# Kernel tuning notes

Measured on AMD Instinct MI355X. Metric: run time of the kernel, lower is better.

The kernel has to match this reference:

```python
import jax, jax.numpy as jnp
import numpy as np

D_MODEL = 768
N_HEADS = 24
D_HEAD = 64
D_STATE = 64
CHUNK = 64
D_INNER = N_HEADS * D_HEAD  # 1536
N_LAYER = 24
B_SZ = 2
SEQ = 8192
RMS_EPS = 1.1920929e-07  # torch.finfo(float32).eps (nn.RMSNorm default eps)


def setup_inputs() -> dict:
    key = jax.random.key(0)
    ks = jax.random.split(key, 8)
    proj = N_HEADS * (1 + 2 * D_STATE)
    return {
        "hidden_states": jax.random.normal(ks[0], (B_SZ, SEQ, D_MODEL), jnp.float32),
        "norm_w": jnp.ones((D_MODEL,), jnp.float32),
        "in_proj_w": jax.random.normal(ks[1], (2 * D_INNER, D_MODEL), jnp.float32) * 0.02,
        "in_proj_b": jnp.zeros((2 * D_INNER,), jnp.float32),
        "conv_w": jax.random.normal(ks[2], (D_INNER, 1, 4), jnp.float32) * 0.25,
        "conv_b": jnp.zeros((D_INNER,), jnp.float32),
        "x_proj_w": jax.random.normal(ks[3], (proj, D_INNER), jnp.float32) * 0.02,
        "x_proj_b": jnp.zeros((proj,), jnp.float32),
        "A_log": jnp.full((N_HEADS,), float(np.log(0.5)), jnp.float32),
        "log2_alpha_base": jnp.full((N_HEADS,), -0.15, jnp.float32),
        "log2_beta": jnp.zeros((N_HEADS,), jnp.float32),
        "surprise_ema": jnp.ones((N_HEADS,), jnp.float32),
        "out_proj_w": jax.random.normal(ks[4], (D_MODEL, D_INNER), jnp.float32) * 0.02,
        "out_proj_b": jnp.zeros((D_MODEL,), jnp.float32),
        "res_gate": jnp.full((1,), 1.0 / float(np.sqrt(2 * N_LAYER)), jnp.float32),
    }


def _block_forward(hidden_states, norm_w, in_proj_w, in_proj_b, conv_w, conv_b,
                   x_proj_w, x_proj_b, A_log, log2_alpha_base, log2_beta,
                   surprise_ema, out_proj_w, out_proj_b, res_gate):
    residual = hidden_states
    b, L, _ = hidden_states.shape

    # RMSNorm
    x = hidden_states * jax.lax.rsqrt(
        jnp.mean(hidden_states ** 2, axis=-1, keepdims=True) + RMS_EPS) * norm_w

    # in_proj, split x/z
    xz = hidden_states_proj = x @ in_proj_w.T + in_proj_b
    x, z = jnp.split(xz, 2, axis=-1)  # [b, L, d_inner] each

    # causal depthwise conv1d (kernel 4, padding 3, then truncate to L)
    xc = jnp.transpose(x, (0, 2, 1))  # [b, C, L]
    xc = jax.lax.conv_general_dilated(
        xc, conv_w, window_strides=(1,), padding=[(3, 3)],
        dimension_numbers=("NCH", "OIH", "NCH"), feature_group_count=D_INNER)
    xc = xc[:, :, :L] + conv_b[None, :, None]
    x = jax.nn.silu(jnp.transpose(xc, (0, 2, 1)))  # [b, L, d_inner]

    # x_proj -> dt, B, C
    xp = (x @ x_proj_w.T + x_proj_b).reshape(b, L, N_HEADS, 1 + 2 * D_STATE)
    dt = xp[..., 0]
    B_ssm = xp[..., 1:1 + D_STATE]
    C_ssm = xp[..., 1 + D_STATE:]
    B_ssm = B_ssm / jnp.maximum(jnp.linalg.norm(B_ssm, axis=-1, keepdims=True), 1e-12)
    C_ssm = C_ssm / jnp.maximum(jnp.linalg.norm(C_ssm, axis=-1, keepdims=True), 1e-12)

    A = jnp.clip(A_log, -2.3, -0.01)[None, None, :]  # [1,1,H]
    dt_scale = jnp.clip(jax.nn.softplus(jnp.clip(dt, -10.0, 10.0)), 0.01, 10.0)
    A = jnp.clip(A * dt_scale, -20.0, -0.001)  # [b, L, H]

    X = x.reshape(b, L, N_HEADS, D_HEAD)

    # ---- chunked surprise-gated SSD (L divisible by CHUNK) ----
    n = L // CHUNK
    X_t = X.reshape(b, n, CHUNK, N_HEADS, D_HEAD).transpose(0, 3, 1, 2, 4)      # b h n c d
    A_t = A.reshape(b, n, CHUNK, N_HEADS).transpose(0, 3, 1, 2)                 # b h n c
    B_t = B_ssm.reshape(b, n, CHUNK, N_HEADS, D_STATE).transpose(0, 3, 1, 2, 4) # b h n c s
    C_t = C_ssm.reshape(b, n, CHUNK, N_HEADS, D_STATE).transpose(0, 3, 1, 2, 4) # b h n c s

    BX = jnp.einsum("bhncs,bhncd->bhnsd", B_t, X_t)
    chunk_surprise = jnp.mean(BX ** 2, axis=(-1, -2))  # [b, h, n]

    # surprise gate (training=True: EMA updated first, no_grad)
    mean_s = jax.lax.stop_gradient(jnp.mean(chunk_surprise, axis=(0, 2)))
    ema = 0.99 * surprise_ema + 0.01 * mean_s
    normalized = chunk_surprise / (ema[None, :, None] + 1e-6)
    alpha_base = 1.0 - 2.0 ** jnp.clip(log2_alpha_base, -3.32, -0.015)  # [H]
    beta = 2.0 ** jnp.clip(log2_beta, -2.0, 2.0)                        # [H]
    boost_pos = jax.nn.relu(jnp.tanh(beta[None, :, None] * normalized))
    ab = alpha_base[None, :, None]
    alpha = jnp.clip(ab + (1.0 - ab) * boost_pos, 0.01, 0.999)          # [b, h, n]

    A_mod = A_t * (1.0 - alpha)[..., None]          # b h n c
    A_cs = jnp.cumsum(A_mod, axis=-1)               # b h n c

    # intra-chunk: L[i,j] = exp(cs_i - cs_j) for i >= j
    diff = A_cs[..., :, None] - A_cs[..., None, :]  # b h n c c
    mask = jnp.tril(jnp.ones((CHUNK, CHUNK), bool))
    Lmat = jnp.where(mask, jnp.exp(diff), 0.0)
    CB = jnp.einsum("bhnid,bhnjd->bhnij", C_t, B_t)
    Y_intra = jnp.einsum("bhnij,bhnjd->bhnid", Lmat * CB, X_t)

    # inter-chunk recurrence
    decay_chunk = jnp.exp(jnp.sum(A_mod, axis=-1))              # b h n
    decay_to_end = jnp.exp(A_cs[..., -1:] - A_cs)               # b h n c
    h_chunk_final = jnp.einsum("bhnc,bhncs,bhncd->bhnsd",
                               decay_to_end, B_t, X_t)           # b h n s d

    def step(carry, inp):
        d, hf = inp  # d: [b,h], hf: [b,h,s,d]
        new = d[..., None, None] * carry + hf
        return new, carry  # emit state BEFORE this chunk

    carry0 = jnp.zeros((b, N_HEADS, D_STATE, D_HEAD), X.dtype)
    _, h_inter = jax.lax.scan(
        step, carry0,
        (decay_chunk.transpose(2, 0, 1), h_chunk_final.transpose(2, 0, 1, 3, 4)))
    h_inter = h_inter.transpose(1, 2, 0, 3, 4)  # b h n s d

    decay_from_start = jnp.exp(A_cs)  # b h n c
    Y_inter = jnp.einsum("bhnis,bhnsp,bhni->bhnip", C_t, h_inter, decay_from_start)

    Y = (Y_intra + Y_inter).transpose(0, 2, 3, 1, 4).reshape(b, L, D_INNER)

    # gate + out proj + gated residual
    y = jnp.clip(Y, -100.0, 100.0) * jax.nn.sigmoid(z)
    out = jnp.clip(y @ out_proj_w.T + out_proj_b, -100.0, 100.0)
    return residual + out * res_gate


def reference(hidden_states, norm_w, in_proj_w, in_proj_b, conv_w, conv_b,
              x_proj_w, x_proj_b, A_log, log2_alpha_base, log2_beta,
              surprise_ema, out_proj_w, out_proj_b, res_gate):
    return _block_forward(hidden_states, norm_w, in_proj_w, in_proj_b, conv_w,
                          conv_b, x_proj_w, x_proj_b, A_log, log2_alpha_base,
                          log2_beta, surprise_ema, out_proj_w, out_proj_b, res_gate)
```

## Files before the change

kernel.cpp:

```cpp
#include <hip/hip_runtime.h>
#include <hip/hip_bf16.h>
#include <cstdint>
#include <cstddef>

#define L_SEQ   8192
#define DMODEL  768
#define NHEADS  24
#define DINNER  1536
#define NPROJ   3096
#define NPROJP  3200
#define NTOK    16384
#define SEG_T   4096
#define NSEG    4
#define SEG_CH  64
#define RMS_EPS 1.1920929e-07f

typedef __hip_bfloat16 bf16;
typedef __attribute__((ext_vector_type(8))) short bf8v;
typedef __attribute__((ext_vector_type(4))) float f4v;

__device__ __forceinline__ float clampf(float x, float lo, float hi) {
    return fminf(fmaxf(x, lo), hi);
}
__device__ __forceinline__ float bf2f(bf16 v) { return __bfloat162float(v); }
__device__ __forceinline__ bf16  f2bf(float v) { return __float2bfloat16(v); }
__device__ __forceinline__ short f2bs(float v) {
    bf16 b = __float2bfloat16(v);
    return *reinterpret_cast<short*>(&b);
}
__device__ __forceinline__ void st1(float* p, float v) { *p = v; }
__device__ __forceinline__ void st1(bf16* p, float v) { *p = f2bf(v); }
__device__ __forceinline__ void st4(float* p, float4 v) { *(float4*)p = v; }
__device__ __forceinline__ void st4(bf16* p, float4 v) {
    p[0] = f2bf(v.x); p[1] = f2bf(v.y); p[2] = f2bf(v.z); p[3] = f2bf(v.w);
}

#define GLOAD16(gsrc, ldst) __builtin_amdgcn_global_load_lds( \
    (const __attribute__((address_space(1))) void*)(gsrc),    \
    (__attribute__((address_space(3))) void*)(ldst), 16, 0, 0)

__global__ __launch_bounds__(256) void k_cvt(const float* __restrict__ s,
                                             bf16* __restrict__ d, int n4) {
    int i = blockIdx.x * 256 + threadIdx.x;
    if (i < n4) {
        float4 v = *(const float4*)&s[i * 4];
        st4(&d[i * 4], v);
    }
}
__global__ __launch_bounds__(256) void k_zero(bf16* __restrict__ d, int n) {
    int i = blockIdx.x * 256 + threadIdx.x;
    if (i < n) d[i] = f2bf(0.f);
}

__global__ __launch_bounds__(256) void k_rmsnorm(const float* __restrict__ hs,
                                                 const float* __restrict__ w,
                                                 bf16* __restrict__ xn) {
    int t = blockIdx.x;
    const float* p = hs + (size_t)t * DMODEL;
    float s = 0.f;
    for (int i = threadIdx.x; i < DMODEL; i += 256) { float v = p[i]; s += v * v; }
    for (int off = 32; off; off >>= 1) s += __shfl_xor(s, off, 64);
    __shared__ float ws4[4];
    int lane = threadIdx.x & 63, wv = threadIdx.x >> 6;
    if (lane == 0) ws4[wv] = s;
    __syncthreads();
    s = ws4[0] + ws4[1] + ws4[2] + ws4[3];
    float r = 1.0f / sqrtf(s * (1.0f / DMODEL) + RMS_EPS);
    bf16* o = xn + (size_t)t * DMODEL;
    for (int i = threadIdx.x; i < DMODEL; i += 256) o[i] = f2bf(p[i] * r * w[i]);
}

template <typename TC, int EPI>
__global__ __launch_bounds__(256) void k_mgemm(const bf16* __restrict__ A,
                                               const bf16* __restrict__ B,
                                               const float* __restrict__ bias,
                                               TC* __restrict__ C,
                                               int M, int N, int K,
                                               const float* __restrict__ resid,
                                               const float* __restrict__ gatep,
                                               bf16* __restrict__ halo) {
    __shared__ short As[2][128 * 32];
    __shared__ short Bs[2][128 * 32];
    int tid = threadIdx.x;
    int lane = tid & 63, w = tid >> 6;

    int gx = gridDim.x, gy = gridDim.y;
    int bid = blockIdx.y * gx + blockIdx.x;
    int xcd = bid & 7, idx = bid >> 3;
    int bys = gy >> 3;
    int gby = bys < 8 ? bys : 8;
    int sg  = idx / (gx * gby);
    int rem = idx - sg * (gx * gby);
    int bx  = rem / gby;
    int byl = rem - bx * gby;
    int by  = xcd * bys + sg * gby + byl;
    int m0 = by * 128, n0 = bx * 128;

    int wm = (w >> 1) << 6, wn = (w & 1) << 6;

    const size_t rowskip = (size_t)16 * K * 2;
    const char* Ag = (const char*)(A + (size_t)(m0 + (w << 5) + (lane >> 2)) * K) + (lane & 3) * 16;
    const char* Bg = (const char*)(B + (size_t)(n0 + (w << 5) + (lane >> 2)) * K) + (lane & 3) * 16;
    short* Al0 = &As[0][(w << 5) * 32];
    short* Bl0 = &Bs[0][(w << 5) * 32];
    short* Al1 = &As[1][(w << 5) * 32];
    short* Bl1 = &Bs[1][(w << 5) * 32];

    f4v acc[4][4];
#pragma unroll
    for (int i = 0; i < 4; ++i)
#pragma unroll
        for (int j = 0; j < 4; ++j) acc[i][j] = (f4v){0.f, 0.f, 0.f, 0.f};

    auto stage = [&](int buf, int k0) {
        size_t kb = (size_t)k0 * 2;
        short* Al = buf ? Al1 : Al0;
        short* Bl = buf ? Bl1 : Bl0;
        GLOAD16(Ag + kb,           Al);
        GLOAD16(Ag + kb + rowskip, Al + 16 * 32);
        GLOAD16(Bg + kb,           Bl);
        GLOAD16(Bg + kb + rowskip, Bl + 16 * 32);
    };

    stage(0, 0);
    int cur = 0;
    int row16 = lane & 15, kg = (lane >> 4) << 3;
    for (int k0 = 0; k0 < K; k0 += 32) {
        __syncthreads();
        if (k0 + 32 < K) stage(cur ^ 1, k0 + 32);
        const short* Ab = As[cur];
        const short* Bb = Bs[cur];
        bf8v af[4], bfv[4];
#pragma unroll
        for (int fm = 0; fm < 4; ++fm)
            af[fm] = *(const bf8v*)&Ab[(wm + (fm << 4) + row16) * 32 + kg];
#pragma unroll
        for (int fn = 0; fn < 4; ++fn)
            bfv[fn] = *(const bf8v*)&Bb[(wn + (fn << 4) + row16) * 32 + kg];
#pragma unroll
        for (int fm = 0; fm < 4; ++fm)
#pragma unroll
            for (int fn = 0; fn < 4; ++fn)
                acc[fm][fn] = __builtin_amdgcn_mfma_f32_16x16x32_bf16(
                    af[fm], bfv[fn], acc[fm][fn], 0, 0, 0);
        cur ^= 1;
    }

    float gate = (EPI == 1) ? *gatep : 0.f;
    int rbase = m0 + wm + ((lane >> 4) << 2);
#pragma unroll
    for (int fn = 0; fn < 4; ++fn) {
        int col = n0 + wn + (fn << 4) + (lane & 15);
        if (col >= N) continue;
        float bc = bias[col];
#pragma unroll
        for (int fm = 0; fm < 4; ++fm) {
#pragma unroll
            for (int r = 0; r < 4; ++r) {
                int row = rbase + (fm << 4) + r;
                float v = acc[fm][fn][r] + bc;
                if (EPI == 1)
                    v = resid[(size_t)row * N + col] + clampf(v, -100.f, 100.f) * gate;
                st1(&C[(size_t)row * N + col], v);
                if (halo && row >= M - 3)
                    halo[(size_t)(row - (M - 3)) * N + col] = f2bf(v);
            }
        }
    }
}

__global__ __launch_bounds__(256) void k_conv_silu(const bf16* __restrict__ x,
                                                   const bf16* __restrict__ xh,
                                                   const float* __restrict__ cw,
                                                   const float* __restrict__ cb,
                                                   bf16* __restrict__ xc,
                                                   int l0) {
    int c = blockIdx.x * 256 + threadIdx.x;
    int r = blockIdx.y;
    int l = l0 + r;
    float acc = cb[c];
#pragma unroll
    for (int k = 0; k < 4; ++k) {
        int lp = l - 3 + k;
        if (lp < 0) continue;
        float v = (lp < l0) ? bf2f(xh[(size_t)(lp - l0 + 3) * DINNER + c])
                            : bf2f(x[(size_t)(lp - l0) * DINNER + c]);
        acc += cw[c * 4 + k] * v;
    }
    float sig = 1.f / (1.f + expf(-acc));
    xc[(size_t)r * DINNER + c] = f2bf(acc * sig);
}

__global__ __launch_bounds__(256) void k_prep(const bf16* __restrict__ xp,
                                              const float* __restrict__ A_log,
                                              float* __restrict__ Aarr,
                                              float* __restrict__ invB,
                                              float* __restrict__ invC) {
    int wv = threadIdx.x >> 6, lane = threadIdx.x & 63;
    int idx = blockIdx.x * 4 + wv;
    int t = idx / 24, h = idx - t * 24;
    const bf16* base = xp + (size_t)t * NPROJ + h * 129;
    float b = bf2f(base[1 + lane]), c = bf2f(base[65 + lane]);
    float sb = b * b, sc = c * c;
    for (int off = 32; off; off >>= 1) {
        sb += __shfl_xor(sb, off, 64);
        sc += __shfl_xor(sc, off, 64);
    }
    if (lane == 0) {
        invB[idx] = 1.f / fmaxf(sqrtf(sb), 1e-12f);
        invC[idx] = 1.f / fmaxf(sqrtf(sc), 1e-12f);
        float dt = clampf(bf2f(base[0]), -10.f, 10.f);
        float dts = clampf(log1pf(expf(dt)), 0.01f, 10.f);
        float A = clampf(A_log[h], -2.3f, -0.01f) * dts;
        Aarr[idx] = clampf(A, -20.f, -0.001f);
    }
}

__device__ __forceinline__ void surprise_body(const bf16* xp, const bf16* xc,
                                              const float* invB, float* cs,
                                              int t0, int h, size_t cs_idx) {
    __shared__ short Ws[64 * 72];
    __shared__ short Xt[64 * 72];
    int tid = threadIdx.x, s = tid & 63, cg = tid >> 6;
    for (int it = 0; it < 16; ++it) {
        int c = cg + (it << 2);
        int t = t0 + c;
        Ws[s * 72 + c] = f2bs(bf2f(xp[(size_t)t * NPROJ + h * 129 + 1 + s]) * invB[t * 24 + h]);
        Xt[s * 72 + c] = *(const short*)&xc[(size_t)t * DINNER + h * 64 + s];
    }
    __syncthreads();
    int w = tid >> 6, lane = tid & 63;
    int r16 = lane & 15, kq = (lane >> 4) << 3;
    int strip = w << 4;
    f4v acc[4];
#pragma unroll
    for (int dt = 0; dt < 4; ++dt) acc[dt] = (f4v){0.f, 0.f, 0.f, 0.f};
#pragma unroll
    for (int ks = 0; ks < 2; ++ks) {
        bf8v af = *(const bf8v*)&Ws[(strip + r16) * 72 + ks * 32 + kq];
#pragma unroll
        for (int dt = 0; dt < 4; ++dt) {
            bf8v bf_ = *(const bf8v*)&Xt[((dt << 4) + r16) * 72 + ks * 32 + kq];
            acc[dt] = __builtin_amdgcn_mfma_f32_16x16x32_bf16(af, bf_, acc[dt], 0, 0, 0);
        }
    }
    float ss = 0.f;
#pragma unroll
    for (int dt = 0; dt < 4; ++dt)
#pragma unroll
        for (int r = 0; r < 4; ++r) ss += acc[dt][r] * acc[dt][r];
    for (int off = 32; off; off >>= 1) ss += __shfl_xor(ss, off, 64);
    __shared__ float ws4[4];
    if (lane == 0) ws4[w] = ss;
    __syncthreads();
    if (tid == 0) cs[cs_idx] = (ws4[0] + ws4[1] + ws4[2] + ws4[3]) * (1.f / 4096.f);
}

__global__ __launch_bounds__(256) void k_surprise(const bf16* __restrict__ xp,
                                                  const bf16* __restrict__ xc,
                                                  const float* __restrict__ invB,
                                                  float* __restrict__ cs,
                                                  int b, int l0) {
    int g = blockIdx.x;
    int h = g >> 6, nl = g & 63;
    surprise_body(xp, xc, invB, cs, nl * 64, h,
                  (size_t)(b * 24 + h) * 128 + (l0 >> 6) + nl);
}

__global__ __launch_bounds__(256) void k_surprise_all(const bf16* __restrict__ xp,
                                                      const bf16* __restrict__ xc,
                                                      const float* __restrict__ invB,
                                                      float* __restrict__ cs) {
    int g = blockIdx.x;
    int cg = g / 24, h = g - cg * 24;
    int b = cg >> 7, nl = cg & 127;
    surprise_body(xp, xc, invB, cs, cg * 64, h, (size_t)(b * 24 + h) * 128 + nl);
}

__global__ __launch_bounds__(256) void k_alpha(const float* __restrict__ cs,
                                               const float* __restrict__ ema0,
                                               const float* __restrict__ l2ab,
                                               const float* __restrict__ l2b,
                                               float* __restrict__ alpha) {
    int h = blockIdx.x, tid = threadIdx.x;
    int b = tid >> 7, n = tid & 127;
    int gi = (b * 24 + h) * 128 + n;
    float v = cs[gi];
    float s = v;
    for (int off = 32; off; off >>= 1) s += __shfl_xor(s, off, 64);
    __shared__ float ws4[4];
    int lane = tid & 63, wv = tid >> 6;
    if (lane == 0) ws4[wv] = s;
    __syncthreads();
    float total = ws4[0] + ws4[1] + ws4[2] + ws4[3];
    float ema = 0.99f * ema0[h] + 0.01f * (total * (1.f / 256.f));
    float ab = 1.f - exp2f(clampf(l2ab[h], -3.32f, -0.015f));
    float beta = exp2f(clampf(l2b[h], -2.f, 2.f));
    float nz = v / (ema + 1e-6f);
    float boost = fmaxf(tanhf(beta * nz), 0.f);
    alpha[gi] = clampf(ab + (1.f - ab) * boost, 0.01f, 0.999f);
}

__global__ __launch_bounds__(256) void k_chunk(const bf16* __restrict__ xp,
                                               const bf16* __restrict__ xc,
                                               const float* __restrict__ invB,
                                               const float* __restrict__ invC,
                                               const float* __restrict__ Aarr,
                                               const float* __restrict__ alpha,
                                               bf16* __restrict__ ybuf,
                                               bf16* __restrict__ hf,
                                               float* __restrict__ dchunk,
                                               int b, int l0, int lognch) {
    int g = blockIdx.x;
    int h = g >> lognch, nl = g & ((1 << lognch) - 1);
    int t0l = nl * 64;
    size_t gidx = (size_t)(b * 24 + h) * 128 + (l0 >> 6) + nl;
    float alp = alpha[gidx];
    __shared__ short Cs[64 * 72];
    __shared__ short Bs[64 * 72];
    __shared__ short Ws[64 * 72];
    __shared__ short Xt[64 * 72];
    __shared__ float Acs[64];
    __shared__ float dte[64];
    int tid = threadIdx.x;
    if (tid < 64) {
        float a = Aarr[(size_t)(t0l + tid) * 24 + h] * (1.f - alp);
        for (int off = 1; off < 64; off <<= 1) {
            float u = __shfl_up(a, off, 64);
            if (tid >= off) a += u;
        }
        Acs[tid] = a;
        float total = __shfl(a, 63, 64);
        dte[tid] = expf(total - a);
        if (tid == 0) dchunk[gidx] = expf(total);
    }
    __syncthreads();
    int s = tid & 63, cg = tid >> 6;
    for (int it = 0; it < 16; ++it) {
        int c = cg + (it << 2);
        int t = t0l + c;
        const bf16* bp = xp + (size_t)t * NPROJ + h * 129;
        float bv = bf2f(bp[1 + s]) * invB[t * 24 + h];
        Bs[c * 72 + s] = f2bs(bv);
        Ws[s * 72 + c] = f2bs(bv * dte[c]);
        Cs[c * 72 + s] = f2bs(bf2f(bp[65 + s]) * invC[t * 24 + h]);
        Xt[s * 72 + c] = *(const short*)&xc[(size_t)t * DINNER + h * 64 + s];
    }
    __syncthreads();
    int w = tid >> 6, lane = tid & 63;
    int r16 = lane & 15, kq = (lane >> 4) << 3;
    int strip = w << 4;
    f4v acb[4], ach[4];
#pragma unroll
    for (int jt = 0; jt < 4; ++jt) {
        acb[jt] = (f4v){0.f, 0.f, 0.f, 0.f};
        ach[jt] = (f4v){0.f, 0.f, 0.f, 0.f};
    }
#pragma unroll
    for (int ks = 0; ks < 2; ++ks) {
        bf8v afc = *(const bf8v*)&Cs[(strip + r16) * 72 + ks * 32 + kq];
        bf8v afw = *(const bf8v*)&Ws[(strip + r16) * 72 + ks * 32 + kq];
#pragma unroll
        for (int jt = 0; jt < 4; ++jt) {
            bf8v bb = *(const bf8v*)&Bs[((jt << 4) + r16) * 72 + ks * 32 + kq];
            acb[jt] = __builtin_amdgcn_mfma_f32_16x16x32_bf16(afc, bb, acb[jt], 0, 0, 0);
            bf8v xx = *(const bf8v*)&Xt[((jt << 4) + r16) * 72 + ks * 32 + kq];
            ach[jt] = __builtin_amdgcn_mfma_f32_16x16x32_bf16(afw, xx, ach[jt], 0, 0, 0);
        }
    }
    size_t hbase = (size_t)((h << lognch) + nl) * 4096;
    int rbase = strip + ((lane >> 4) << 2);
#pragma unroll
    for (int dt = 0; dt < 4; ++dt) {
        int d = (dt << 4) + r16;
#pragma unroll
        for (int r = 0; r < 4; ++r)
            hf[hbase + (size_t)(rbase + r) * 64 + d] = f2bf(ach[dt][r]);
    }
    __syncthreads();
    short* Ms = Cs;
#pragma unroll
    for (int jt = 0; jt < 4; ++jt) {
        int j = (jt << 4) + r16;
        float aj = Acs[j];
#pragma unroll
        for (int r = 0; r < 4; ++r) {
            int i = rbase + r;
            float m = (j <= i) ? expf(Acs[i] - aj) * acb[jt][r] : 0.f;
            Ms[i * 72 + j] = f2bs(m);
        }
    }
    __syncthreads();
    f4v acy[4];
#pragma unroll
    for (int dt = 0; dt < 4; ++dt) acy[dt] = (f4v){0.f, 0.f, 0.f, 0.f};
#pragma unroll
    for (int ks = 0; ks < 2; ++ks) {
        bf8v afm = *(const bf8v*)&Ms[(strip + r16) * 72 + ks * 32 + kq];
#pragma unroll
        for (int dt = 0; dt < 4; ++dt) {
            bf8v xx = *(const bf8v*)&Xt[((dt << 4) + r16) * 72 + ks * 32 + kq];
            acy[dt] = __builtin_amdgcn_mfma_f32_16x16x32_bf16(afm, xx, acy[dt], 0, 0, 0);
        }
    }
#pragma unroll
    for (int dt = 0; dt < 4; ++dt) {
        int d = (dt << 4) + r16;
#pragma unroll
        for (int r = 0; r < 4; ++r) {
            int i = rbase + r;
            ybuf[(size_t)(t0l + i) * DINNER + h * 64 + d] = f2bf(acy[dt][r]);
        }
    }
}

__global__ __launch_bounds__(256) void k_scan(bf16* __restrict__ hf,
                                              const float* __restrict__ dchunk,
                                              float* __restrict__ carry,
                                              int b, int l0, int nch) {
    int h = blockIdx.x >> 4;
    int e = ((blockIdx.x & 15) << 8) + threadIdx.x;
    int bh = b * 24 + h;
    float c = (l0 == 0) ? 0.f : carry[(size_t)bh * 4096 + e];
    size_t a = (size_t)h * nch * 4096 + e;
    float v = bf2f(hf[a]);
    const float* dcp = dchunk + (size_t)bh * 128 + (l0 >> 6);
    for (int nl = 0; nl < nch; ++nl) {
        float dc = dcp[nl];
        float vn = (nl + 1 < nch) ? bf2f(hf[a + 4096]) : 0.f;
        hf[a] = f2bf(c);
        c = dc * c + v;
        v = vn;
        a += 4096;
    }
    carry[(size_t)bh * 4096 + e] = c;
}

__global__ __launch_bounds__(256) void k_inter(const bf16* __restrict__ xp,
                                               const float* __restrict__ invC,
                                               const float* __restrict__ Aarr,
                                               const float* __restrict__ alpha,
                                               const bf16* __restrict__ hf,
                                               const bf16* __restrict__ zbuf,
                                               bf16* __restrict__ ybuf,
                                               int b, int l0, int lognch) {
    int g = blockIdx.x;
    int h = g >> lognch, nl = g & ((1 << lognch) - 1);
    int t0l = nl * 64;
    float alp = alpha[(size_t)(b * 24 + h) * 128 + (l0 >> 6) + nl];
    __shared__ short Cs[64 * 72];
    __shared__ short Ht[64 * 72];
    __shared__ float dfs[64];
    int tid = threadIdx.x;
    if (tid < 64) {
        float a = Aarr[(size_t)(t0l + tid) * 24 + h] * (1.f - alp);
        for (int off = 1; off < 64; off <<= 1) {
            float u = __shfl_up(a, off, 64);
            if (tid >= off) a += u;
        }
        dfs[tid] = expf(a);
    }
    int s = tid & 63, cg = tid >> 6;
    size_t hbase = (size_t)((h << lognch) + nl) * 4096;
    for (int it = 0; it < 16; ++it) {
        int c = cg + (it << 2);
        int t = t0l + c;
        Cs[c * 72 + s] = f2bs(bf2f(xp[(size_t)t * NPROJ + h * 129 + 65 + s]) * invC[t * 24 + h]);
        Ht[s * 72 + c] = *(const short*)&hf[hbase + (size_t)c * 64 + s];
    }
    __syncthreads();
    int w = tid >> 6, lane = tid & 63;
    int r16 = lane & 15, kq = (lane >> 4) << 3;
    int strip = w << 4;
    f4v acc[4];
#pragma unroll
    for (int dt = 0; dt < 4; ++dt) acc[dt] = (f4v){0.f, 0.f, 0.f, 0.f};
#pragma unroll
    for (int ks = 0; ks < 2; ++ks) {
        bf8v af = *(const bf8v*)&Cs[(strip + r16) * 72 + ks * 32 + kq];
#pragma unroll
        for (int dt = 0; dt < 4; ++dt) {
            bf8v hfr = *(const bf8v*)&Ht[((dt << 4) + r16) * 72 + ks * 32 + kq];
            acc[dt] = __builtin_amdgcn_mfma_f32_16x16x32_bf16(af, hfr, acc[dt], 0, 0, 0);
        }
    }
    int ibase = strip + ((lane >> 4) << 2);
#pragma unroll
    for (int dt = 0; dt < 4; ++dt) {
        int d = (dt << 4) + r16;
#pragma unroll
        for (int r = 0; r < 4; ++r) {
            int i = ibase + r;
            float df = dfs[i];
            size_t yoff = (size_t)(t0l + i) * DINNER + h * 64 + d;
            float Y = clampf(bf2f(ybuf[yoff]) + df * acc[dt][r], -100.f, 100.f);
            float zz = bf2f(zbuf[yoff]);
            ybuf[yoff] = f2bf(Y / (1.f + expf(-zz)));
        }
    }
}

extern "C" void kernel_launch(void* const* d_in, const int* in_sizes, int n_in,
                              void* d_out, int out_size, void* d_ws, size_t ws_size,
                              hipStream_t stream) {
    const float* hs     = (const float*)d_in[0];
    const float* norm_w = (const float*)d_in[1];
    const float* w1     = (const float*)d_in[2];
    const float* b1     = (const float*)d_in[3];
    const float* cw     = (const float*)d_in[4];
    const float* cbias  = (const float*)d_in[5];
    const float* w2     = (const float*)d_in[6];
    const float* b2     = (const float*)d_in[7];
    const float* A_log  = (const float*)d_in[8];
    const float* l2ab   = (const float*)d_in[9];
    const float* l2b    = (const float*)d_in[10];
    const float* ema0   = (const float*)d_in[11];
    const float* w3     = (const float*)d_in[12];
    const float* b3     = (const float*)d_in[13];
    const float* rg     = (const float*)d_in[14];
    float* out = (float*)d_out;

    const bool BATCH = ws_size >= (size_t)200 * 1000 * 1000;
    const bool BIG   = BATCH || ws_size >= (size_t)172 * 1024 * 1024;

    char* base = (char*)d_ws;
    size_t off = 0;
    auto alloc = [&](size_t bytes) -> void* {
        void* p = base + off;
        off += (bytes + 255) & ~(size_t)255;
        return p;
    };
    const size_t YROWS = BATCH ? 8192 : SEG_T;
    const int    NCH   = BATCH ? 128 : SEG_CH;
    bf16* w1bf  = (bf16*)alloc((size_t)2 * DINNER * DMODEL * 2);
    bf16* w2bf  = (bf16*)alloc((size_t)NPROJP * DINNER * 2);
    bf16* w3bf  = (bf16*)alloc((size_t)DMODEL * DINNER * 2);
    bf16* xn    = (bf16*)alloc((size_t)NTOK * DMODEL * 2);
    bf16* ybuf  = (bf16*)alloc(YROWS * DINNER * 2);
    bf16* hf    = (bf16*)alloc((size_t)NHEADS * NCH * 4096 * 2);
    bf16* xhalo = (bf16*)alloc((size_t)2 * 3 * DINNER * 2);
    float* cs   = (float*)alloc((size_t)6144 * 4);
    float* alp  = (float*)alloc((size_t)6144 * 4);
    float* dch  = (float*)alloc((size_t)6144 * 4);
    float* carry= (float*)alloc((size_t)48 * 4096 * 4);
    size_t ntokA = BIG ? (size_t)NTOK : (size_t)SEG_T;
    bf16* xp    = (bf16*)alloc(ntokA * NPROJ * 2);
    float* Aarr = (float*)alloc(ntokA * 24 * 4);
    float* invB = (float*)alloc(ntokA * 24 * 4);
    float* invC = (float*)alloc(ntokA * 24 * 4);
    bf16* xbuf  = ybuf;
    bf16* xc_all = (bf16*)d_out;

    {
        int n1 = 2 * DINNER * DMODEL / 4, n2 = NPROJ * DINNER / 4, n3 = DMODEL * DINNER / 4;
        k_cvt<<<(n1 + 255) / 256, 256, 0, stream>>>(w1, w1bf, n1);
        k_cvt<<<(n2 + 255) / 256, 256, 0, stream>>>(w2, w2bf, n2);
        k_cvt<<<(n3 + 255) / 256, 256, 0, stream>>>(w3, w3bf, n3);
        int nz = (NPROJP - NPROJ) * DINNER;
        k_zero<<<(nz + 255) / 256, 256, 0, stream>>>(w2bf + (size_t)NPROJ * DINNER, nz);
    }

    const dim3 gPall(NPROJP / 128, NTOK / 128);

    if (BATCH) {
        const dim3 gXb(DINNER / 128, 8192 / 128);
        const dim3 gOb(DMODEL / 128, 8192 / 128);
        k_rmsnorm<<<NTOK, 256, 0, stream>>>(hs, norm_w, xn);
        for (int bt = 0; bt < 2; ++bt) {
            size_t t0 = (size_t)bt * 8192;
            k_mgemm<bf16, 0><<<gXb, 256, 0, stream>>>(xn + t0 * DMODEL, w1bf, b1, xbuf,
                                                      8192, DINNER, DMODEL, nullptr, nullptr, nullptr);
            k_conv_silu<<<dim3(DINNER / 256, 8192), 256, 0, stream>>>(
                xbuf, xhalo, cw, cbias, xc_all + t0 * DINNER, 0);
        }
        k_mgemm<bf16, 0><<<gPall, 256, 0, stream>>>(xc_all, w2bf, b2, xp,
                                                    NTOK, NPROJ, DINNER, nullptr, nullptr, nullptr);
        k_prep<<<NTOK * 24 / 4, 256, 0, stream>>>(xp, A_log, Aarr, invB, invC);
        k_surprise_all<<<6144, 256, 0, stream>>>(xp, xc_all, invB, cs);
        k_alpha<<<24, 256, 0, stream>>>(cs, ema0, l2ab, l2b, alp);

        for (int bt = 0; bt < 2; ++bt) {
            size_t t0 = (size_t)bt * 8192;
            bf16* xc = xc_all + t0 * DINNER;
            bf16* zseg = xc;
            const bf16* xpS = xp + t0 * NPROJ;
            const float* AarrS = Aarr + t0 * 24;
            const float* invBS = invB + t0 * 24;
            const float* invCS = invC + t0 * 24;
            k_chunk<<<NHEADS * 128, 256, 0, stream>>>(xpS, xc, invBS, invCS, AarrS, alp,
                                                      ybuf, hf, dch, bt, 0, 7);
            k_mgemm<bf16, 0><<<gXb, 256, 0, stream>>>(xn + t0 * DMODEL,
                                                      w1bf + (size_t)DINNER * DMODEL,
                                                      b1 + DINNER, zseg,
                                                      8192, DINNER, DMODEL, nullptr, nullptr, nullptr);
            k_scan<<<384, 256, 0, stream>>>(hf, dch, carry, bt, 0, 128);
            k_inter<<<NHEADS * 128, 256, 0, stream>>>(xpS, invCS, AarrS, alp, hf, zseg,
                                                      ybuf, bt, 0, 7);
            k_mgemm<float, 1><<<gOb, 256, 0, stream>>>(ybuf, w3bf, b3, out + t0 * DMODEL,
                                                       8192, DMODEL, DINNER,
                                                       hs + t0 * DMODEL, rg, nullptr);
        }
        return;
    }

    const dim3 gX(DINNER / 128, SEG_T / 128);
    const dim3 gP(NPROJP / 128, SEG_T / 128);
    const dim3 gO(DMODEL / 128, SEG_T / 128);

    k_rmsnorm<<<NTOK, 256, 0, stream>>>(hs, norm_w, xn);
    for (int s = 0; s < NSEG; ++s) {
        size_t t0 = (size_t)s * SEG_T;
        int l0 = (int)(t0 & (L_SEQ - 1));
        bf16* xc = xc_all + t0 * DINNER;
        k_mgemm<bf16, 0><<<gX, 256, 0, stream>>>(xn + t0 * DMODEL, w1bf, b1, xbuf,
                                                 SEG_T, DINNER, DMODEL, nullptr, nullptr,
                                                 xhalo + (size_t)((s + 1) & 1) * 3 * DINNER);
        k_conv_silu<<<dim3(DINNER / 256, SEG_T), 256, 0, stream>>>(
            xbuf, xhalo + (size_t)(s & 1) * 3 * DINNER, cw, cbias, xc, l0);
        if (!BIG) {
            int b = (int)(t0 >> 13);
            k_mgemm<bf16, 0><<<gP, 256, 0, stream>>>(xc, w2bf, b2, xp,
                                                     SEG_T, NPROJ, DINNER, nullptr, nullptr, nullptr);
            k_prep<<<SEG_T * 24 / 4, 256, 0, stream>>>(xp, A_log, Aarr, invB, invC);
            k_surprise<<<NHEADS * SEG_CH, 256, 0, stream>>>(xp, xc, invB, cs, b, l0);
        }
    }
    if (BIG) {
        k_mgemm<bf16, 0><<<gPall, 256, 0, stream>>>(xc_all, w2bf, b2, xp,
                                                    NTOK, NPROJ, DINNER, nullptr, nullptr, nullptr);
        k_prep<<<NTOK * 24 / 4, 256, 0, stream>>>(xp, A_log, Aarr, invB, invC);
        k_surprise_all<<<6144, 256, 0, stream>>>(xp, xc_all, invB, cs);
    }
    k_alpha<<<24, 256, 0, stream>>>(cs, ema0, l2ab, l2b, alp);

    for (int s = 0; s < NSEG; ++s) {
        size_t t0 = (size_t)s * SEG_T;
        int l0 = (int)(t0 & (L_SEQ - 1));
        int b  = (int)(t0 >> 13);
        const float* hseg = hs + t0 * DMODEL;
        bf16* xc = xc_all + t0 * DINNER;
        bf16* zseg = xc;
        const bf16* xpS;
        const float* AarrS;
        const float* invBS;
        const float* invCS;
        if (BIG) {
            xpS   = xp   + t0 * NPROJ;
            AarrS = Aarr + t0 * 24;
            invBS = invB + t0 * 24;
            invCS = invC + t0 * 24;
        } else {
            k_mgemm<bf16, 0><<<gP, 256, 0, stream>>>(xc, w2bf, b2, xp,
                                                     SEG_T, NPROJ, DINNER, nullptr, nullptr, nullptr);
            k_prep<<<SEG_T * 24 / 4, 256, 0, stream>>>(xp, A_log, Aarr, invB, invC);
            xpS = xp; AarrS = Aarr; invBS = invB; invCS = invC;
        }
        k_chunk<<<NHEADS * SEG_CH, 256, 0, stream>>>(xpS, xc, invBS, invCS, AarrS, alp,
                                                     ybuf, hf, dch, b, l0, 6);
        k_mgemm<bf16, 0><<<gX, 256, 0, stream>>>(xn + t0 * DMODEL,
                                                 w1bf + (size_t)DINNER * DMODEL,
                                                 b1 + DINNER, zseg,
                                                 SEG_T, DINNER, DMODEL, nullptr, nullptr, nullptr);
        k_scan<<<384, 256, 0, stream>>>(hf, dch, carry, b, l0, SEG_CH);
        k_inter<<<NHEADS * SEG_CH, 256, 0, stream>>>(xpS, invCS, AarrS, alp, hf, zseg,
                                                     ybuf, b, l0, 6);
        k_mgemm<float, 1><<<gO, 256, 0, stream>>>(ybuf, w3bf, b3, out + t0 * DMODEL,
                                                  SEG_T, DMODEL, DINNER, hseg, rg, nullptr);
    }
}
```

Measured before the change: 967.8 us.

## Process full batch in single launches and vectorize causal conv

The BIG path now runs the in-projection, conv, chunk, z-projection, scan, inter and out-projection kernels once over all 16384 tokens instead of looping per batch. New k_chunk_all, k_scan_all and k_inter_all kernels cover both batches. The conv kernel reads whole rows with 8-wide bf16 vector loads and drops the halo buffer written from the GEMM epilogue. The non-BIG path drops its 4096-token segmentation in favour of per-batch segments. The intent is fewer launches, larger grids and less per-segment overhead, at the cost of larger intermediate buffers.

```diff
diff --git a/kernel.cpp b/kernel.cpp
--- a/kernel.cpp
+++ b/kernel.cpp
@@ -10,9 +10,6 @@
 #define NPROJ   3096
 #define NPROJP  3200
 #define NTOK    16384
-#define SEG_T   4096
-#define NSEG    4
-#define SEG_CH  64
 #define RMS_EPS 1.1920929e-07f
 
 typedef __hip_bfloat16 bf16;
@@ -28,9 +25,11 @@
     bf16 b = __float2bfloat16(v);
     return *reinterpret_cast<short*>(&b);
 }
+__device__ __forceinline__ float bs2f(short v) {
+    return __uint_as_float(((unsigned)(unsigned short)v) << 16);
+}
 __device__ __forceinline__ void st1(float* p, float v) { *p = v; }
 __device__ __forceinline__ void st1(bf16* p, float v) { *p = f2bf(v); }
-__device__ __forceinline__ void st4(float* p, float4 v) { *(float4*)p = v; }
 __device__ __forceinline__ void st4(bf16* p, float4 v) {
     p[0] = f2bf(v.x); p[1] = f2bf(v.y); p[2] = f2bf(v.z); p[3] = f2bf(v.w);
 }
@@ -77,8 +76,7 @@
                                                TC* __restrict__ C,
                                                int M, int N, int K,
                                                const float* __restrict__ resid,
-                                               const float* __restrict__ gatep,
-                                               bf16* __restrict__ halo) {
+                                               const float* __restrict__ gatep) {
     __shared__ short As[2][128 * 32];
     __shared__ short Bs[2][128 * 32];
     int tid = threadIdx.x;
@@ -162,33 +160,38 @@
                 if (EPI == 1)
                     v = resid[(size_t)row * N + col] + clampf(v, -100.f, 100.f) * gate;
                 st1(&C[(size_t)row * N + col], v);
-                if (halo && row >= M - 3)
-                    halo[(size_t)(row - (M - 3)) * N + col] = f2bf(v);
             }
         }
     }
 }
 
-__global__ __launch_bounds__(256) void k_conv_silu(const bf16* __restrict__ x,
-                                                   const bf16* __restrict__ xh,
-                                                   const float* __restrict__ cw,
-                                                   const float* __restrict__ cb,
-                                                   bf16* __restrict__ xc,
-                                                   int l0) {
-    int c = blockIdx.x * 256 + threadIdx.x;
-    int r = blockIdx.y;
-    int l = l0 + r;
-    float acc = cb[c];
+__global__ __launch_bounds__(192) void k_conv8(const bf16* __restrict__ x,
+                                               const float* __restrict__ cw,
+                                               const float* __restrict__ cb,
+                                               bf16* __restrict__ xc) {
+    int c0 = threadIdx.x * 8;
+    int r  = blockIdx.x;
+    int l  = r & (L_SEQ - 1);
+    float acc[8];
+#pragma unroll
+    for (int j = 0; j < 8; ++j) acc[j] = cb[c0 + j];
 #pragma unroll
     for (int k = 0; k < 4; ++k) {
         int lp = l - 3 + k;
         if (lp < 0) continue;
-        float v = (lp < l0) ? bf2f(xh[(size_t)(lp - l0 + 3) * DINNER + c])
-                            : bf2f(x[(size_t)(lp - l0) * DINNER + c]);
-        acc += cw[c * 4 + k] * v;
-    }
-    float sig = 1.f / (1.f + expf(-acc));
-    xc[(size_t)r * DINNER + c] = f2bf(acc * sig);
+        const short* px = (const short*)(x + (size_t)(r - 3 + k) * DINNER + c0);
+        bf8v v = *(const bf8v*)px;
+#pragma unroll
+        for (int j = 0; j < 8; ++j)
+            acc[j] += cw[(c0 + j) * 4 + k] * bs2f(v[j]);
+    }
+    bf8v o;
+#pragma unroll
+    for (int j = 0; j < 8; ++j) {
+        float a = acc[j];
+        o[j] = f2bs(a / (1.f + expf(-a)));
+    }
+    *(bf8v*)(xc + (size_t)r * DINNER + c0) = o;
 }
 
 __global__ __launch_bounds__(256) void k_prep(const bf16* __restrict__ xp,
@@ -216,57 +219,6 @@
     }
 }
 
-__device__ __forceinline__ void surprise_body(const bf16* xp, const bf16* xc,
-                                              const float* invB, float* cs,
-                                              int t0, int h, size_t cs_idx) {
-    __shared__ short Ws[64 * 72];
-    __shared__ short Xt[64 * 72];
-    int tid = threadIdx.x, s = tid & 63, cg = tid >> 6;
-    for (int it = 0; it < 16; ++it) {
-        int c = cg + (it << 2);
-        int t = t0 + c;
-        Ws[s * 72 + c] = f2bs(bf2f(xp[(size_t)t * NPROJ + h * 129 + 1 + s]) * invB[t * 24 + h]);
-        Xt[s * 72 + c] = *(const short*)&xc[(size_t)t * DINNER + h * 64 + s];
-    }
-    __syncthreads();
-    int w = tid >> 6, lane = tid & 63;
-    int r16 = lane & 15, kq = (lane >> 4) << 3;
-    int strip = w << 4;
-    f4v acc[4];
-#pragma unroll
-    for (int dt = 0; dt < 4; ++dt) acc[dt] = (f4v){0.f, 0.f, 0.f, 0.f};
-#pragma unroll
-    for (int ks = 0; ks < 2; ++ks) {
-        bf8v af = *(const bf8v*)&Ws[(strip + r16) * 72 + ks * 32 + kq];
-#pragma unroll
-        for (int dt = 0; dt < 4; ++dt) {
-            bf8v bf_ = *(const bf8v*)&Xt[((dt << 4) + r16) * 72 + ks * 32 + kq];
-            acc[dt] = __builtin_amdgcn_mfma_f32_16x16x32_bf16(af, bf_, acc[dt], 0, 0, 0);
-        }
-    }
-    float ss = 0.f;
-#pragma unroll
-    for (int dt = 0; dt < 4; ++dt)
-#pragma unroll
-        for (int r = 0; r < 4; ++r) ss += acc[dt][r] * acc[dt][r];
-    for (int off = 32; off; off >>= 1) ss += __shfl_xor(ss, off, 64);
-    __shared__ float ws4[4];
-    if (lane == 0) ws4[w] = ss;
-    __syncthreads();
-    if (tid == 0) cs[cs_idx] = (ws4[0] + ws4[1] + ws4[2] + ws4[3]) * (1.f / 4096.f);
-}
-
-__global__ __launch_bounds__(256) void k_surprise(const bf16* __restrict__ xp,
-                                                  const bf16* __restrict__ xc,
-                                                  const float* __restrict__ invB,
-                                                  float* __restrict__ cs,
-                                                  int b, int l0) {
-    int g = blockIdx.x;
-    int h = g >> 6, nl = g & 63;
-    surprise_body(xp, xc, invB, cs, nl * 64, h,
-                  (size_t)(b * 24 + h) * 128 + (l0 >> 6) + nl);
-}
-
 __global__ __launch_bounds__(256) void k_surprise_all(const bf16* __restrict__ xp,
                                                       const bf16* __restrict__ xc,
                                                       const float* __restrict__ invB,
@@ -274,7 +226,43 @@
     int g = blockIdx.x;
     int cg = g / 24, h = g - cg * 24;
     int b = cg >> 7, nl = cg & 127;
-    surprise_body(xp, xc, invB, cs, cg * 64, h, (size_t)(b * 24 + h) * 128 + nl);
+    int t0 = cg * 64;
+    size_t cs_idx = (size_t)(b * 24 + h) * 128 + nl;
+    __shared__ short Ws[64 * 72];
+    __shared__ short Xt[64 * 72];
+    int tid = threadIdx.x, s = tid & 63, cg2 = tid >> 6;
+    for (int it = 0; it < 16; ++it) {
+        int c = cg2 + (it << 2);
+        int t = t0 + c;
+        Ws[s * 72 + c] = f2bs(bf2f(xp[(size_t)t * NPROJ + h * 129 + 1 + s]) * invB[t * 24 + h]);
+        Xt[s * 72 + c] = *(const short*)&xc[(size_t)t * DINNER + h * 64 + s];
+    }
+    __syncthreads();
+    int w = tid >> 6, lane = tid & 63;
+    int r16 = lane & 15, kq = (lane >> 4) << 3;
+    int strip = w << 4;
+    f4v acc[4];
+#pragma unroll
+    for (int dt = 0; dt < 4; ++dt) acc[dt] = (f4v){0.f, 0.f, 0.f, 0.f};
+#pragma unroll
+    for (int ks = 0; ks < 2; ++ks) {
+        bf8v af = *(const bf8v*)&Ws[(strip + r16) * 72 + ks * 32 + kq];
+#pragma unroll
+        for (int dt = 0; dt < 4; ++dt) {
+            bf8v bf_ = *(const bf8v*)&Xt[((dt << 4) + r16) * 72 + ks * 32 + kq];
+            acc[dt] = __builtin_amdgcn_mfma_f32_16x16x32_bf16(af, bf_, acc[dt], 0, 0, 0);
+        }
+    }
+    float ss = 0.f;
+#pragma unroll
+    for (int dt = 0; dt < 4; ++dt)
+#pragma unroll
+        for (int r = 0; r < 4; ++r) ss += acc[dt][r] * acc[dt][r];
+    for (int off = 32; off; off >>= 1) ss += __shfl_xor(ss, off, 64);
+    __shared__ float ws4[4];
+    if (lane == 0) ws4[w] = ss;
+    __syncthreads();
+    if (tid == 0) cs[cs_idx] = (ws4[0] + ws4[1] + ws4[2] + ws4[3]) * (1.f / 4096.f);
 }
 
 __global__ __launch_bounds__(256) void k_alpha(const float* __restrict__ cs,
@@ -301,6 +289,109 @@
     alpha[gi] = clampf(ab + (1.f - ab) * boost, 0.01f, 0.999f);
 }
 
+__device__ __forceinline__ void chunk_body(const bf16* xp, const bf16* xc,
+                                           const float* invB, const float* invC,
+                                           const float* Aarr, const float* alpha,
+                                           bf16* ybuf, bf16* hf, float* dchunk,
+                                           int t0, int h, size_t gidx, size_t hbase) {
+    float alp = alpha[gidx];
+    __shared__ short Cs[64 * 72];
+    __shared__ short Bs[64 * 72];
+    __shared__ short Ws[64 * 72];
+    __shared__ short Xt[64 * 72];
+    __shared__ float Acs[64];
+    __shared__ float dte[64];
+    int tid = threadIdx.x;
+    if (tid < 64) {
+        float a = Aarr[(size_t)(t0 + tid) * 24 + h] * (1.f - alp);
+        for (int off = 1; off < 64; off <<= 1) {
+            float u = __shfl_up(a, off, 64);
+            if (tid >= off) a += u;
+        }
+        Acs[tid] = a;
+        float total = __shfl(a, 63, 64);
+        dte[tid] = expf(total - a);
+        if (tid == 0) dchunk[gidx] = expf(total);
+    }
+    __syncthreads();
+    int s = tid & 63, cg = tid >> 6;
+    for (int it = 0; it < 16; ++it) {
+        int c = cg + (it << 2);
+        int t = t0 + c;
+        const bf16* bp = xp + (size_t)t * NPROJ + h * 129;
+        float bv = bf2f(bp[1 + s]) * invB[t * 24 + h];
+        Bs[c * 72 + s] = f2bs(bv);
+        Ws[s * 72 + c] = f2bs(bv * dte[c]);
+        Cs[c * 72 + s] = f2bs(bf2f(bp[65 + s]) * invC[t * 24 + h]);
+        Xt[s * 72 + c] = *(const short*)&xc[(size_t)t * DINNER + h * 64 + s];
+    }
+    __syncthreads();
+    int w = tid >> 6, lane = tid & 63;
+    int r16 = lane & 15, kq = (lane >> 4) << 3;
+    int strip = w << 4;
+    f4v acb[4], ach[4];
+#pragma unroll
+    for (int jt = 0; jt < 4; ++jt) {
+        acb[jt] = (f4v){0.f, 0.f, 0.f, 0.f};
+        ach[jt] = (f4v){0.f, 0.f, 0.f, 0.f};
+    }
+#pragma unroll
+    for (int ks = 0; ks < 2; ++ks) {
+        bf8v afc = *(const bf8v*)&Cs[(strip + r16) * 72 + ks * 32 + kq];
+        bf8v afw = *(const bf8v*)&Ws[(strip + r16) * 72 + ks * 32 + kq];
+#pragma unroll
+        for (int jt = 0; jt < 4; ++jt) {
+            bf8v bb = *(const bf8v*)&Bs[((jt << 4) + r16) * 72 + ks * 32 + kq];
+            acb[jt] = __builtin_amdgcn_mfma_f32_16x16x32_bf16(afc, bb, acb[jt], 0, 0, 0);
+            bf8v xx = *(const bf8v*)&Xt[((jt << 4) + r16) * 72 + ks * 32 + kq];
+            ach[jt] = __builtin_amdgcn_mfma_f32_16x16x32_bf16(afw, xx, ach[jt], 0, 0, 0);
+        }
+    }
+    int rbase = strip + ((lane >> 4) << 2);
+#pragma unroll
+    for (int dt = 0; dt < 4; ++dt) {
+        int d = (dt << 4) + r16;
+#pragma unroll
+        for (int r = 0; r < 4; ++r)
+            hf[hbase + (size_t)(rbase + r) * 64 + d] = f2bf(ach[dt][r]);
+    }
+    __syncthreads();
+    short* Ms = Cs;
+#pragma unroll
+    for (int jt = 0; jt < 4; ++jt) {
+        int j = (jt << 4) + r16;
+        float aj = Acs[j];
+#pragma unroll
+        for (int r = 0; r < 4; ++r) {
+            int i = rbase + r;
+            float m = (j <= i) ? expf(Acs[i] - aj) * acb[jt][r] : 0.f;
+            Ms[i * 72 + j] = f2bs(m);
+        }
+    }
+    __syncthreads();
+    f4v acy[4];
+#pragma unroll
+    for (int dt = 0; dt < 4; ++dt) acy[dt] = (f4v){0.f, 0.f, 0.f, 0.f};
+#pragma unroll
+    for (int ks = 0; ks < 2; ++ks) {
+        bf8v afm = *(const bf8v*)&Ms[(strip + r16) * 72 + ks * 32 + kq];
+#pragma unroll
+        for (int dt = 0; dt < 4; ++dt) {
+            bf8v xx = *(const bf8v*)&Xt[((dt << 4) + r16) * 72 + ks * 32 + kq];
+            acy[dt] = __builtin_amdgcn_mfma_f32_16x16x32_bf16(afm, xx, acy[dt], 0, 0, 0);
+        }
+    }
+#pragma unroll
+    for (int dt = 0; dt < 4; ++dt) {
+        int d = (dt << 4) + r16;
+#pragma unroll
+        for (int r = 0; r < 4; ++r) {
+            int i = rbase + r;
+            ybuf[(size_t)(t0 + i) * DINNER + h * 64 + d] = f2bf(acy[dt][r]);
+        }
+    }
+}
+
 __global__ __launch_bounds__(256) void k_chunk(const bf16* __restrict__ xp,
                                                const bf16* __restrict__ xc,
                                                const float* __restrict__ invB,
@@ -313,105 +404,27 @@
                                                int b, int l0, int lognch) {
     int g = blockIdx.x;
     int h = g >> lognch, nl = g & ((1 << lognch) - 1);
-    int t0l = nl * 64;
-    size_t gidx = (size_t)(b * 24 + h) * 128 + (l0 >> 6) + nl;
-    float alp = alpha[gidx];
-    __shared__ short Cs[64 * 72];
-    __shared__ short Bs[64 * 72];
-    __shared__ short Ws[64 * 72];
-    __shared__ short Xt[64 * 72];
-    __shared__ float Acs[64];
-    __shared__ float dte[64];
-    int tid = threadIdx.x;
-    if (tid < 64) {
-        float a = Aarr[(size_t)(t0l + tid) * 24 + h] * (1.f - alp);
-        for (int off = 1; off < 64; off <<= 1) {
-            float u = __shfl_up(a, off, 64);
-            if (tid >= off) a += u;
-        }
-        Acs[tid] = a;
-        float total = __shfl(a, 63, 64);
-        dte[tid] = expf(total - a);
-        if (tid == 0) dchunk[gidx] = expf(total);
-    }
-    __syncthreads();
-    int s = tid & 63, cg = tid >> 6;
-    for (int it = 0; it < 16; ++it) {
-        int c = cg + (it << 2);
-        int t = t0l + c;
-        const bf16* bp = xp + (size_t)t * NPROJ + h * 129;
-        float bv = bf2f(bp[1 + s]) * invB[t * 24 + h];
-        Bs[c * 72 + s] = f2bs(bv);
-        Ws[s * 72 + c] = f2bs(bv * dte[c]);
-        Cs[c * 72 + s] = f2bs(bf2f(bp[65 + s]) * invC[t * 24 + h]);
-        Xt[s * 72 + c] = *(const short*)&xc[(size_t)t * DINNER + h * 64 + s];
-    }
-    __syncthreads();
-    int w = tid >> 6, lane = tid & 63;
-    int r16 = lane & 15, kq = (lane >> 4) << 3;
-    int strip = w << 4;
-    f4v acb[4], ach[4];
-#pragma unroll
-    for (int jt = 0; jt < 4; ++jt) {
-        acb[jt] = (f4v){0.f, 0.f, 0.f, 0.f};
-        ach[jt] = (f4v){0.f, 0.f, 0.f, 0.f};
-    }
-#pragma unroll
-    for (int ks = 0; ks < 2; ++ks) {
-        bf8v afc = *(const bf8v*)&Cs[(strip + r16) * 72 + ks * 32 + kq];
-        bf8v afw = *(const bf8v*)&Ws[(strip + r16) * 72 + ks * 32 + kq];
-#pragma unroll
-        for (int jt = 0; jt < 4; ++jt) {
-            bf8v bb = *(const bf8v*)&Bs[((jt << 4) + r16) * 72 + ks * 32 + kq];
-            acb[jt] = __builtin_amdgcn_mfma_f32_16x16x32_bf16(afc, bb, acb[jt], 0, 0, 0);
-            bf8v xx = *(const bf8v*)&Xt[((jt << 4) + r16) * 72 + ks * 32 + kq];
-            ach[jt] = __builtin_amdgcn_mfma_f32_16x16x32_bf16(afw, xx, ach[jt], 0, 0, 0);
-        }
-    }
-    size_t hbase = (size_t)((h << lognch) + nl) * 4096;
-    int rbase = strip + ((lane >> 4) << 2);
-#pragma unroll
-    for (int dt = 0; dt < 4; ++dt) {
-        int d = (dt << 4) + r16;
-#pragma unroll
-        for (int r = 0; r < 4; ++r)
-            hf[hbase + (size_t)(rbase + r) * 64 + d] = f2bf(ach[dt][r]);
-    }
-    __syncthreads();
-    short* Ms = Cs;
-#pragma unroll
-    for (int jt = 0; jt < 4; ++jt) {
-        int j = (jt << 4) + r16;
-        float aj = Acs[j];
-#pragma unroll
-        for (int r = 0; r < 4; ++r) {
-            int i = rbase + r;
-            float m = (j <= i) ? expf(Acs[i] - aj) * acb[jt][r] : 0.f;
-            Ms[i * 72 + j] = f2bs(m);
-        }
-    }
-    __syncthreads();
-    f4v acy[4];
-#pragma unroll
-    for (int dt = 0; dt < 4; ++dt) acy[dt] = (f4v){0.f, 0.f, 0.f, 0.f};
-#pragma unroll
-    for (int ks = 0; ks < 2; ++ks) {
-        bf8v afm = *(const bf8v*)&Ms[(strip + r16) * 72 + ks * 32 + kq];
-#pragma unroll
-        for (int dt = 0; dt < 4; ++dt) {
-            bf8v xx = *(const bf8v*)&Xt[((dt << 4) + r16) * 72 + ks * 32 + kq];
-            acy[dt] = __builtin_amdgcn_mfma_f32_16x16x32_bf16(afm, xx, acy[dt], 0, 0, 0);
-        }
-    }
-#pragma unroll
-    for (int dt = 0; dt < 4; ++dt) {
-        int d = (dt << 4) + r16;
-#pragma unroll
-        for (int r = 0; r < 4; ++r) {
-            int i = rbase + r;
-            ybuf[(size_t)(t0l + i) * DINNER + h * 64 + d] = f2bf(acy[dt][r]);
-        }
-    }
+    chunk_body(xp, xc, invB, invC, Aarr, alpha, ybuf, hf, dchunk,
+               nl * 64, h,
+               (size_t)(b * 24 + h) * 128 + (l0 >> 6) + nl,
+               (size_t)((h << lognch) + nl) * 4096);
+}
+
+__global__ __launch_bounds__(256) void k_chunk_all(const bf16* __restrict__ xp,
+                                                   const bf16* __restrict__ xc,
+                                                   const float* __restrict__ invB,
+                                                   const float* __restrict__ invC,
+                                                   const float* __restrict__ Aarr,
+                                                   const float* __restrict__ alpha,
+                                                   bf16* __restrict__ ybuf,
+                                                   bf16* __restrict__ hf,
+                                                   float* __restrict__ dchunk) {
+    int g = blockIdx.x;
+    int bh = g >> 7, nl = g & 127;
+    int b = bh >= 24 ? 1 : 0, h = bh - b * 24;
+    size_t gidx = (size_t)bh * 128 + nl;
+    chunk_body(xp, xc, invB, invC, Aarr, alpha, ybuf, hf, dchunk,
+               b * L_SEQ + nl * 64, h, gidx, gidx * 4096);
 }
 
 __global__ __launch_bounds__(256) void k_scan(bf16* __restrict__ hf,
@@ -436,6 +449,81 @@
     carry[(size_t)bh * 4096 + e] = c;
 }
 
+__global__ __launch_bounds__(256) void k_scan_all(bf16* __restrict__ hf,
+                                                  const float* __restrict__ dchunk) {
+    int bh = blockIdx.x >> 4;
+    int e = ((blockIdx.x & 15) << 8) + threadIdx.x;
+    float c = 0.f;
+    size_t a = (size_t)bh * 128 * 4096 + e;
+    float v = bf2f(hf[a]);
+    const float* dcp = dchunk + (size_t)bh * 128;
+    for (int nl = 0; nl < 128; ++nl) {
+        float dc = dcp[nl];
+        float vn = (nl + 1 < 128) ? bf2f(hf[a + 4096]) : 0.f;
+        hf[a] = f2bf(c);
+        c = dc * c + v;
+        v = vn;
+        a += 4096;
+    }
+}
+
+__device__ __forceinline__ void inter_body(const bf16* xp, const float* invC,
+                                           const float* Aarr, const float* alpha,
+                                           const bf16* hf, const bf16* zbuf,
+                                           bf16* ybuf,
+                                           int t0, int h, size_t gidx, size_t hbase) {
+    float alp = alpha[gidx];
+    __shared__ short Cs[64 * 72];
+    __shared__ short Ht[64 * 72];
+    __shared__ float dfs[64];
+    int tid = threadIdx.x;
+    if (tid < 64) {
+        float a = Aarr[(size_t)(t0 + tid) * 24 + h] * (1.f - alp);
+        for (int off = 1; off < 64; off <<= 1) {
+            float u = __shfl_up(a, off, 64);
+            if (tid >= off) a += u;
+        }
+        dfs[tid] = expf(a);
+    }
+    int s = tid & 63, cg = tid >> 6;
+    for (int it = 0; it < 16; ++it) {
+        int c = cg + (it << 2);
+        int t = t0 + c;
+        Cs[c * 72 + s] = f2bs(bf2f(xp[(size_t)t * NPROJ + h * 129 + 65 + s]) * invC[t * 24 + h]);
+        Ht[s * 72 + c] = *(const short*)&hf[hbase + (size_t)c * 64 + s];
+    }
+    __syncthreads();
+    int w = tid >> 6, lane = tid & 63;
+    int r16 = lane & 15, kq = (lane >> 4) << 3;
+    int strip = w << 4;
+    f4v acc[4];
+#pragma unroll
+    for (int dt = 0; dt < 4; ++dt) acc[dt] = (f4v){0.f, 0.f, 0.f, 0.f};
+#pragma unroll
+    for (int ks = 0; ks < 2; ++ks) {
+        bf8v af = *(const bf8v*)&Cs[(strip + r16) * 72 + ks * 32 + kq];
+#pragma unroll
+        for (int dt = 0; dt < 4; ++dt) {
+            bf8v hfr = *(const bf8v*)&Ht[((dt << 4) + r16) * 72 + ks * 32 + kq];
+            acc[dt] = __builtin_amdgcn_mfma_f32_16x16x32_bf16(af, hfr, acc[dt], 0, 0, 0);
+        }
+    }
+    int ibase = strip + ((lane >> 4) << 2);
+#pragma unroll
+    for (int dt = 0; dt < 4; ++dt) {
+        int d = (dt << 4) + r16;
+#pragma unroll
+        for (int r = 0; r < 4; ++r) {
+            int i = ibase + r;
+            float df = dfs[i];
+            size_t yoff = (size_t)(t0 + i) * DINNER + h * 64 + d;
+            float Y = clampf(bf2f(ybuf[yoff]) + df * acc[dt][r], -100.f, 100.f);
+            float zz = bf2f(zbuf[yoff]);
+            ybuf[yoff] = f2bf(Y / (1.f + expf(-zz)));
+        }
+    }
+}
+
 __global__ __launch_bounds__(256) void k_inter(const bf16* __restrict__ xp,
                                                const float* __restrict__ invC,
                                                const float* __restrict__ Aarr,
@@ -446,58 +534,25 @@
                                                int b, int l0, int lognch) {
     int g = blockIdx.x;
     int h = g >> lognch, nl = g & ((1 << lognch) - 1);
-    int t0l = nl * 64;
-    float alp = alpha[(size_t)(b * 24 + h) * 128 + (l0 >> 6) + nl];
-    __shared__ short Cs[64 * 72];
-    __shared__ short Ht[64 * 72];
-    __shared__ float dfs[64];
-    int tid = threadIdx.x;
-    if (tid < 64) {
-        float a = Aarr[(size_t)(t0l + tid) * 24 + h] * (1.f - alp);
-        for (int off = 1; off < 64; off <<= 1) {
-            float u = __shfl_up(a, off, 64);
-            if (tid >= off) a += u;
-        }
-        dfs[tid] = expf(a);
-    }
-    int s = tid & 63, cg = tid >> 6;
-    size_t hbase = (size_t)((h << lognch) + nl) * 4096;
-    for (int it = 0; it < 16; ++it) {
-        int c = cg + (it << 2);
-        int t = t0l + c;
-        Cs[c * 72 + s] = f2bs(bf2f(xp[(size_t)t * NPROJ + h * 129 + 65 + s]) * invC[t * 24 + h]);
-        Ht[s * 72 + c] = *(const short*)&hf[hbase + (size_t)c * 64 + s];
-    }
-    __syncthreads();
-    int w = tid >> 6, lane = tid & 63;
-    int r16 = lane & 15, kq = (lane >> 4) << 3;
-    int strip = w << 4;
-    f4v acc[4];
-#pragma unroll
-    for (int dt = 0; dt < 4; ++dt) acc[dt] = (f4v){0.f, 0.f, 0.f, 0.f};
-#pragma unroll
-    for (int ks = 0; ks < 2; ++ks) {
-        bf8v af = *(const bf8v*)&Cs[(strip + r16) * 72 + ks * 32 + kq];
-#pragma unroll
-        for (int dt = 0; dt < 4; ++dt) {
-            bf8v hfr = *(const bf8v*)&Ht[((dt << 4) + r16) * 72 + ks * 32 + kq];
-            acc[dt] = __builtin_amdgcn_mfma_f32_16x16x32_bf16(af, hfr, acc[dt], 0, 0, 0);
-        }
-    }
-    int ibase = strip + ((lane >> 4) << 2);
-#pragma unroll
-    for (int dt = 0; dt < 4; ++dt) {
-        int d = (dt << 4) + r16;
-#pragma unroll
-        for (int r = 0; r < 4; ++r) {
-            int i = ibase + r;
-            float df = dfs[i];
-            size_t yoff = (size_t)(t0l + i) * DINNER + h * 64 + d;
-            float Y = clampf(bf2f(ybuf[yoff]) + df * acc[dt][r], -100.f, 100.f);
-            float zz = bf2f(zbuf[yoff]);
-            ybuf[yoff] = f2bf(Y / (1.f + expf(-zz)));
-        }
-    }
+    inter_body(xp, invC, Aarr, alpha, hf, zbuf, ybuf,
+               nl * 64, h,
+               (size_t)(b * 24 + h) * 128 + (l0 >> 6) + nl,
+               (size_t)((h << lognch) + nl) * 4096);
+}
+
+__global__ __launch_bounds__(256) void k_inter_all(const bf16* __restrict__ xp,
+                                                   const float* __restrict__ invC,
+                                                   const float* __restrict__ Aarr,
+                                                   const float* __restrict__ alpha,
+                                                   const bf16* __restrict__ hf,
+                                                   const bf16* __restrict__ zbuf,
+                                                   bf16* __restrict__ ybuf) {
+    int g = blockIdx.x;
+    int bh = g >> 7, nl = g & 127;
+    int b = bh >= 24 ? 1 : 0, h = bh - b * 24;
+    size_t gidx = (size_t)bh * 128 + nl;
+    inter_body(xp, invC, Aarr, alpha, hf, zbuf, ybuf,
+               b * L_SEQ + nl * 64, h, gidx, gidx * 4096);
 }
 
 extern "C" void kernel_launch(void* const* d_in, const int* in_sizes, int n_in,
@@ -520,8 +575,8 @@
     const float* rg     = (const float*)d_in[14];
     float* out = (float*)d_out;
 
-    const bool BATCH = ws_size >= (size_t)200 * 1000 * 1000;
-    const bool BIG   = BATCH || ws_size >= (size_t)172 * 1024 * 1024;
+    const bool FULL  = ws_size >= (size_t)252 * 1000 * 1000;
+    const int  SEG   = FULL ? NTOK : 8192;
 
     char* base = (char*)d_ws;
     size_t off = 0;
@@ -530,24 +585,20 @@
         off += (bytes + 255) & ~(size_t)255;
         return p;
     };
-    const size_t YROWS = BATCH ? 8192 : SEG_T;
-    const int    NCH   = BATCH ? 128 : SEG_CH;
     bf16* w1bf  = (bf16*)alloc((size_t)2 * DINNER * DMODEL * 2);
     bf16* w2bf  = (bf16*)alloc((size_t)NPROJP * DINNER * 2);
     bf16* w3bf  = (bf16*)alloc((size_t)DMODEL * DINNER * 2);
     bf16* xn    = (bf16*)alloc((size_t)NTOK * DMODEL * 2);
-    bf16* ybuf  = (bf16*)alloc(YROWS * DINNER * 2);
-    bf16* hf    = (bf16*)alloc((size_t)NHEADS * NCH * 4096 * 2);
-    bf16* xhalo = (bf16*)alloc((size_t)2 * 3 * DINNER * 2);
+    bf16* ybuf  = (bf16*)alloc((size_t)SEG * DINNER * 2);
+    bf16* hf    = (bf16*)alloc((size_t)SEG / 64 * NHEADS * 4096 * 2);
     float* cs   = (float*)alloc((size_t)6144 * 4);
     float* alp  = (float*)alloc((size_t)6144 * 4);
     float* dch  = (float*)alloc((size_t)6144 * 4);
     float* carry= (float*)alloc((size_t)48 * 4096 * 4);
-    size_t ntokA = BIG ? (size_t)NTOK : (size_t)SEG_T;
-    bf16* xp    = (bf16*)alloc(ntokA * NPROJ * 2);
-    float* Aarr = (float*)alloc(ntokA * 24 * 4);
-    float* invB = (float*)alloc(ntokA * 24 * 4);
-    float* invC = (float*)alloc(ntokA * 24 * 4);
+    bf16* xp    = (bf16*)alloc((size_t)NTOK * NPROJ * 2);
+    float* Aarr = (float*)alloc((size_t)NTOK * 24 * 4);
+    float* invB = (float*)alloc((size_t)NTOK * 24 * 4);
+    float* invC = (float*)alloc((size_t)NTOK * 24 * 4);
     bf16* xbuf  = ybuf;
     bf16* xc_all = (bf16*)d_out;
 
@@ -562,109 +613,65 @@
 
     const dim3 gPall(NPROJP / 128, NTOK / 128);
 
-    if (BATCH) {
-        const dim3 gXb(DINNER / 128, 8192 / 128);
-        const dim3 gOb(DMODEL / 128, 8192 / 128);
+    if (FULL) {
+        const dim3 gX16(DINNER / 128, NTOK / 128);
+        const dim3 gO16(DMODEL / 128, NTOK / 128);
         k_rmsnorm<<<NTOK, 256, 0, stream>>>(hs, norm_w, xn);
-        for (int bt = 0; bt < 2; ++bt) {
-            size_t t0 = (size_t)bt * 8192;
-            k_mgemm<bf16, 0><<<gXb, 256, 0, stream>>>(xn + t0 * DMODEL, w1bf, b1, xbuf,
-                                                      8192, DINNER, DMODEL, nullptr, nullptr, nullptr);
-            k_conv_silu<<<dim3(DINNER / 256, 8192), 256, 0, stream>>>(
-                xbuf, xhalo, cw, cbias, xc_all + t0 * DINNER, 0);
-        }
+        k_mgemm<bf16, 0><<<gX16, 256, 0, stream>>>(xn, w1bf, b1, xbuf,
+                                                   NTOK, DINNER, DMODEL, nullptr, nullptr);
+        k_conv8<<<NTOK, 192, 0, stream>>>(xbuf, cw, cbias, xc_all);
         k_mgemm<bf16, 0><<<gPall, 256, 0, stream>>>(xc_all, w2bf, b2, xp,
-                                                    NTOK, NPROJ, DINNER, nullptr, nullptr, nullptr);
+                                                    NTOK, NPROJ, DINNER, nullptr, nullptr);
         k_prep<<<NTOK * 24 / 4, 256, 0, stream>>>(xp, A_log, Aarr, invB, invC);
         k_surprise_all<<<6144, 256, 0, stream>>>(xp, xc_all, invB, cs);
         k_alpha<<<24, 256, 0, stream>>>(cs, ema0, l2ab, l2b, alp);
 
-        for (int bt = 0; bt < 2; ++bt) {
-            size_t t0 = (size_t)bt * 8192;
-            bf16* xc = xc_all + t0 * DINNER;
-            bf16* zseg = xc;
-            const bf16* xpS = xp + t0 * NPROJ;
-            const float* AarrS = Aarr + t0 * 24;
-            const float* invBS = invB + t0 * 24;
-            const float* invCS = invC + t0 * 24;
-            k_chunk<<<NHEADS * 128, 256, 0, stream>>>(xpS, xc, invBS, invCS, AarrS, alp,
-                                                      ybuf, hf, dch, bt, 0, 7);
-            k_mgemm<bf16, 0><<<gXb, 256, 0, stream>>>(xn + t0 * DMODEL,
-                                                      w1bf + (size_t)DINNER * DMODEL,
-                                                      b1 + DINNER, zseg,
-                                                      8192, DINNER, DMODEL, nullptr, nullptr, nullptr);
-            k_scan<<<384, 256, 0, stream>>>(hf, dch, carry, bt, 0, 128);
-            k_inter<<<NHEADS * 128, 256, 0, stream>>>(xpS, invCS, AarrS, alp, hf, zseg,
-                                                      ybuf, bt, 0, 7);
-            k_mgemm<float, 1><<<gOb, 256, 0, stream>>>(ybuf, w3bf, b3, out + t0 * DMODEL,
-                                                       8192, DMODEL, DINNER,
-                                                       hs + t0 * DMODEL, rg, nullptr);
-        }
+        k_chunk_all<<<6144, 256, 0, stream>>>(xp, xc_all, invB, invC, Aarr, alp,
+                                              ybuf, hf, dch);
+        k_mgemm<bf16, 0><<<gX16, 256, 0, stream>>>(xn, w1bf + (size_t)DINNER * DMODEL,
+                                                   b1 + DINNER, xc_all,
+                                                   NTOK, DINNER, DMODEL, nullptr, nullptr);
+        k_scan_all<<<768, 256, 0, stream>>>(hf, dch);
+        k_inter_all<<<6144, 256, 0, stream>>>(xp, invC, Aarr, alp, hf, xc_all, ybuf);
+        k_mgemm<float, 1><<<gO16, 256, 0, stream>>>(ybuf, w3bf, b3, out,
+                                                    NTOK, DMODEL, DINNER, hs, rg);
         return;
     }
 
-    const dim3 gX(DINNER / 128, SEG_T / 128);
-    const dim3 gP(NPROJP / 128, SEG_T / 128);
-    const dim3 gO(DMODEL / 128, SEG_T / 128);
-
+    const dim3 gXb(DINNER / 128, 8192 / 128);
+    const dim3 gOb(DMODEL / 128, 8192 / 128);
     k_rmsnorm<<<NTOK, 256, 0, stream>>>(hs, norm_w, xn);
-    for (int s = 0; s < NSEG; ++s) {
-        size_t t0 = (size_t)s * SEG_T;
-        int l0 = (int)(t0 & (L_SEQ - 1));
-        bf16* xc = xc_all + t0 * DINNER;
-        k_mgemm<bf16, 0><<<gX, 256, 0, stream>>>(xn + t0 * DMODEL, w1bf, b1, xbuf,
-                                                 SEG_T, DINNER, DMODEL, nullptr, nullptr,
-                                                 xhalo + (size_t)((s + 1) & 1) * 3 * DINNER);
-        k_conv_silu<<<dim3(DINNER / 256, SEG_T), 256, 0, stream>>>(
-            xbuf, xhalo + (size_t)(s & 1) * 3 * DINNER, cw, cbias, xc, l0);
-        if (!BIG) {
-            int b = (int)(t0 >> 13);
-            k_mgemm<bf16, 0><<<gP, 256, 0, stream>>>(xc, w2bf, b2, xp,
-                                                     SEG_T, NPROJ, DINNER, nullptr, nullptr, nullptr);
-            k_prep<<<SEG_T * 24 / 4, 256, 0, stream>>>(xp, A_log, Aarr, invB, invC);
-            k_surprise<<<NHEADS * SEG_CH, 256, 0, stream>>>(xp, xc, invB, cs, b, l0);
-        }
-    }
-    if (BIG) {
-        k_mgemm<bf16, 0><<<gPall, 256, 0, stream>>>(xc_all, w2bf, b2, xp,
-                                                    NTOK, NPROJ, DINNER, nullptr, nullptr, nullptr);
-        k_prep<<<NTOK * 24 / 4, 256, 0, stream>>>(xp, A_log, Aarr, invB, invC);
-        k_surprise_all<<<6144, 256, 0, stream>>>(xp, xc_all, invB, cs);
-    }
+    for (int bt = 0; bt < 2; ++bt) {
+        size_t t0 = (size_t)bt * 8192;
+        k_mgemm<bf16, 0><<<gXb, 256, 0, stream>>>(xn + t0 * DMODEL, w1bf, b1, xbuf,
+                                                  8192, DINNER, DMODEL, nullptr, nullptr);
+        k_conv8<<<8192, 192, 0, stream>>>(xbuf, cw, cbias, xc_all + t0 * DINNER);
+    }
+    k_mgemm<bf16, 0><<<gPall, 256, 0, stream>>>(xc_all, w2bf, b2, xp,
+                                                NTOK, NPROJ, DINNER, nullptr, nullptr);
+    k_prep<<<NTOK * 24 / 4, 256, 0, stream>>>(xp, A_log, Aarr, invB, invC);
+    k_surprise_all<<<6144, 256, 0, stream>>>(xp, xc_all, invB, cs);
     k_alpha<<<24, 256, 0, stream>>>(cs, ema0, l2ab, l2b, alp);
 
-    for (int s = 0; s < NSEG; ++s) {
-        size_t t0 = (size_t)s * SEG_T;
-        int l0 = (int)(t0 & (L_SEQ - 1));
-        int b  = (int)(t0 >> 13);
-        const float* hseg = hs + t0 * DMODEL;
+    for (int bt = 0; bt < 2; ++bt) {
+        size_t t0 = (size_t)bt * 8192;
         bf16* xc = xc_all + t0 * DINNER;
         bf16* zseg = xc;
-        const bf16* xpS;
-        const float* AarrS;
-        const float* invBS;
-        const float* invCS;
-        if (BIG) {
-            xpS   = xp   + t0 * NPROJ;
-            AarrS = Aarr + t0 * 24;
-            invBS = invB + t0 * 24;
-            invCS = invC + t0 * 24;
-        } else {
-            k_mgemm<bf16, 0><<<gP, 256, 0, stream>>>(xc, w2bf, b2, xp,
-                                                     SEG_T, NPROJ, DINNER, nullptr, nullptr, nullptr);
-            k_prep<<<SEG_T * 24 / 4, 256, 0, stream>>>(xp, A_log, Aarr, invB, invC);
-            xpS = xp; AarrS = Aarr; invBS = invB; invCS = invC;
-        }
-        k_chunk<<<NHEADS * SEG_CH, 256, 0, stream>>>(xpS, xc, invBS, invCS, AarrS, alp,
-                                                     ybuf, hf, dch, b, l0, 6);
-        k_mgemm<bf16, 0><<<gX, 256, 0, stream>>>(xn + t0 * DMODEL,
-                                                 w1bf + (size_t)DINNER * DMODEL,
-                                                 b1 + DINNER, zseg,
-                                                 SEG_T, DINNER, DMODEL, nullptr, nullptr, nullptr);
-        k_scan<<<384, 256, 0, stream>>>(hf, dch, carry, b, l0, SEG_CH);
-        k_inter<<<NHEADS * SEG_CH, 256, 0, stream>>>(xpS, invCS, AarrS, alp, hf, zseg,
-                                                     ybuf, b, l0, 6);
-        k_mgemm<float, 1><<<gO, 256, 0, stream>>>(ybuf, w3bf, b3, out + t0 * DMODEL,
-                                                  SEG_T, DMODEL, DINNER, hseg, rg, nullptr);
-    }
-}
+        const bf16* xpS = xp + t0 * NPROJ;
+        const float* AarrS = Aarr + t0 * 24;
+        const float* invBS = invB + t0 * 24;
+        const float* invCS = invC + t0 * 24;
+        k_chunk<<<NHEADS * 128, 256, 0, stream>>>(xpS, xc, invBS, invCS, AarrS, alp,
+                                                  ybuf, hf, dch, bt, 0, 7);
+        k_mgemm<bf16, 0><<<gXb, 256, 0, stream>>>(xn + t0 * DMODEL,
+                                                  w1bf + (size_t)DINNER * DMODEL,
+                                                  b1 + DINNER, zseg,
+                                                  8192, DINNER, DMODEL, nullptr, nullptr);
+        k_scan<<<384, 256, 0, stream>>>(hf, dch, carry, bt, 0, 128);
+        k_inter<<<NHEADS * 128, 256, 0, stream>>>(xpS, invCS, AarrS, alp, hf, zseg,
+                                                  ybuf, bt, 0, 7);
+        k_mgemm<float, 1><<<gOb, 256, 0, stream>>>(ybuf, w3bf, b3, out + t0 * DMODEL,
+                                                   8192, DMODEL, DINNER,
+                                                   hs + t0 * DMODEL, rg);
+    }
+}
```

After: 979.0 us. Within noise of the previous version (+1.2%).
